# Performance work log

Measured on AMD Instinct MI355X. Metric: run time of the kernel, lower is better.

## Reference

```python
import jax, jax.numpy as jnp
import numpy as np

N = 50000
E = 800000
IN_DIM = 128
OUT_DIM = 128


def setup_inputs() -> dict:
    key = jax.random.key(0)
    k1, k2, k3, k4 = jax.random.split(key, 4)
    x = jax.random.normal(k1, (N, IN_DIM), dtype=jnp.float32)
    edge_index = jax.random.randint(k2, (2, E), 0, N, dtype=jnp.int64)
    # Linear(in_dim*2, out_dim) params
    W = jax.random.normal(k3, (2 * IN_DIM, OUT_DIM), dtype=jnp.float32) * (1.0 / np.sqrt(2 * IN_DIM))
    b = jax.random.normal(k4, (OUT_DIM,), dtype=jnp.float32) * 0.01
    return {"x": x, "edge_index": edge_index, "W": W, "b": b}


def reference(x, edge_index, W, b):
    src, dst = edge_index[0], edge_index[1]
    diff = x[src] - x[dst]                              # (E, C)
    # segment-max over destination nodes; empty segments get -inf identity
    seg_max = jax.ops.segment_max(diff, dst, num_segments=N)  # (N, C)
    counts = jax.ops.segment_sum(jnp.ones((E,), dtype=jnp.int32), dst, num_segments=N)
    # original code leaves zeros for nodes with no incoming edges
    max_diff = jnp.where((counts > 0)[:, None], seg_max, jnp.zeros_like(seg_max))
    x_cat = jnp.concatenate([x, max_diff], axis=-1)     # (N, 2C)
    return x_cat @ W + b
```

## Files before the change

### kernel.cpp

```cpp
#include <hip/hip_runtime.h>
#include <math.h>

#define NN 50000
#define NE 800000
#define CD 128
#define PB 3200

typedef __attribute__((ext_vector_type(8))) short short8;
typedef __attribute__((ext_vector_type(4))) float f32x4;
typedef unsigned long long ull;


__device__ inline unsigned pack2bf(float lo, float hi) {
    unsigned a = __float_as_uint(lo), b = __float_as_uint(hi);
    a = (a + 0x7fffu + ((a >> 16) & 1u)) >> 16;
    b = (b + 0x7fffu + ((b >> 16) & 1u)) & 0xffff0000u;
    return a | b;
}

__device__ inline unsigned short f2bf(float f) {
    unsigned u = __float_as_uint(f);
    return (unsigned short)((u + 0x7fffu + ((u >> 16) & 1u)) >> 16);
}

__device__ inline void fmax8(float* m, uint4 v) {
    m[0] = fmaxf(m[0], __uint_as_float(v.x << 16));
    m[1] = fmaxf(m[1], __uint_as_float(v.x & 0xffff0000u));
    m[2] = fmaxf(m[2], __uint_as_float(v.y << 16));
    m[3] = fmaxf(m[3], __uint_as_float(v.y & 0xffff0000u));
    m[4] = fmaxf(m[4], __uint_as_float(v.z << 16));
    m[5] = fmaxf(m[5], __uint_as_float(v.z & 0xffff0000u));
    m[6] = fmaxf(m[6], __uint_as_float(v.w << 16));
    m[7] = fmaxf(m[7], __uint_as_float(v.w & 0xffff0000u));
}


__global__ __launch_bounds__(256) void prep3_k(const int* __restrict__ ei,
                                               const float* __restrict__ x,
                                               const float* __restrict__ W,
                                               int* __restrict__ head,
                                               ull* __restrict__ nxt2,
                                               unsigned* __restrict__ xb,
                                               unsigned short* __restrict__ wt) {
    int tid0 = blockIdx.x * 256 + threadIdx.x;
    int phase = blockIdx.x & 1;

    for (int p = 0; p < 2; p++) {
        if ((p ^ phase) == 0) {
            for (int e = tid0; e < NE; e += PB * 256) {
                int d = ei[NE + e];
                unsigned s = (unsigned)ei[e];
                int old = atomicExch(&head[d], e);
                nxt2[e] = ((ull)s << 32) | (unsigned)old;
            }
        } else {
            for (int i = tid0; i < NN * CD / 4; i += PB * 256) {
                float4 v = ((const float4*)x)[i];
                uint2 r;
                r.x = pack2bf(v.x, v.y);
                r.y = pack2bf(v.z, v.w);
                ((uint2*)xb)[i] = r;
            }
        }
    }
    for (int i = tid0; i < 2 * CD * CD; i += PB * 256) {
        int n = i >> 8, k = i & 255;
        wt[(size_t)n * 256 + k] = f2bf(W[(size_t)k * 128 + n]);
    }
}


__global__ __launch_bounds__(512) void fused_k(const unsigned* __restrict__ xb,
                                               const int* __restrict__ head,
                                               const ull* __restrict__ nxt2,
                                               const short* __restrict__ wt,
                                               const float* __restrict__ bias,
                                               float* __restrict__ out) {
    __shared__ unsigned short idx[64][72];
    __shared__ unsigned short deg[64];
    __shared__ int ovf[64];
    __shared__ unsigned short amx[64][136];

    int t = threadIdx.x;
    int nbase = blockIdx.x * 64;

    if (t < 64) {
        int node = nbase + t;
        int e = (node < NN) ? head[node] : -1;
        int cnt = 0;
        while (e >= 0 && cnt < 64) {
            ull v = nxt2[e];
            idx[t][cnt] = (unsigned short)(v >> 32);
            e = (int)(unsigned)(v & 0xffffffffu);
            cnt++;
        }
        deg[t] = (unsigned short)cnt;
        ovf[t] = e;
    }
    __syncthreads();

    int w = t >> 6, lane = t & 63;
    int q = lane >> 4, c = lane & 15;
#pragma unroll 1
    for (int j = 0; j < 2; j++) {
        int ln = w * 8 + j * 4 + q;
        int node = nbase + ln;
        int cnt = deg[ln];
        float m[8];
#pragma unroll
        for (int i = 0; i < 8; i++) m[i] = -INFINITY;

        for (int base = 0; base < cnt; base += 8) {
            uint4 pk = *(const uint4*)&idx[ln][base];
            int s0 = (int)(pk.x & 0xffffu), s1 = (int)(pk.x >> 16);
            int s2 = (int)(pk.y & 0xffffu), s3 = (int)(pk.y >> 16);
            int s4 = (int)(pk.z & 0xffffu), s5 = (int)(pk.z >> 16);
            int s6 = (int)(pk.w & 0xffffu), s7 = (int)(pk.w >> 16);
            if (base + 8 <= cnt) {
                fmax8(m, *(const uint4*)(xb + (size_t)s0 * 64 + c * 4));
                fmax8(m, *(const uint4*)(xb + (size_t)s1 * 64 + c * 4));
                fmax8(m, *(const uint4*)(xb + (size_t)s2 * 64 + c * 4));
                fmax8(m, *(const uint4*)(xb + (size_t)s3 * 64 + c * 4));
                fmax8(m, *(const uint4*)(xb + (size_t)s4 * 64 + c * 4));
                fmax8(m, *(const uint4*)(xb + (size_t)s5 * 64 + c * 4));
                fmax8(m, *(const uint4*)(xb + (size_t)s6 * 64 + c * 4));
                fmax8(m, *(const uint4*)(xb + (size_t)s7 * 64 + c * 4));
            } else {
                if (base + 0 < cnt) fmax8(m, *(const uint4*)(xb + (size_t)s0 * 64 + c * 4));
                if (base + 1 < cnt) fmax8(m, *(const uint4*)(xb + (size_t)s1 * 64 + c * 4));
                if (base + 2 < cnt) fmax8(m, *(const uint4*)(xb + (size_t)s2 * 64 + c * 4));
                if (base + 3 < cnt) fmax8(m, *(const uint4*)(xb + (size_t)s3 * 64 + c * 4));
                if (base + 4 < cnt) fmax8(m, *(const uint4*)(xb + (size_t)s4 * 64 + c * 4));
                if (base + 5 < cnt) fmax8(m, *(const uint4*)(xb + (size_t)s5 * 64 + c * 4));
                if (base + 6 < cnt) fmax8(m, *(const uint4*)(xb + (size_t)s6 * 64 + c * 4));
                if (base + 7 < cnt) fmax8(m, *(const uint4*)(xb + (size_t)s7 * 64 + c * 4));
            }
        }
        int e = ovf[ln];
        while (e >= 0) {
            ull v = nxt2[e];
            int s = (int)(v >> 32);
            fmax8(m, *(const uint4*)(xb + (size_t)s * 64 + c * 4));
            e = (int)(unsigned)(v & 0xffffffffu);
        }
        uint4 r = make_uint4(0u, 0u, 0u, 0u);
        if (cnt > 0) {
            uint4 xd = *(const uint4*)(xb + (size_t)node * 64 + c * 4);
            float d0 = m[0] - __uint_as_float(xd.x << 16);
            float d1 = m[1] - __uint_as_float(xd.x & 0xffff0000u);
            float d2 = m[2] - __uint_as_float(xd.y << 16);
            float d3 = m[3] - __uint_as_float(xd.y & 0xffff0000u);
            float d4 = m[4] - __uint_as_float(xd.z << 16);
            float d5 = m[5] - __uint_as_float(xd.z & 0xffff0000u);
            float d6 = m[6] - __uint_as_float(xd.w << 16);
            float d7 = m[7] - __uint_as_float(xd.w & 0xffff0000u);
            r.x = pack2bf(d0, d1);
            r.y = pack2bf(d2, d3);
            r.z = pack2bf(d4, d5);
            r.w = pack2bf(d6, d7);
        }
        *(uint4*)&amx[ln][c * 8] = r;
    }
    __syncthreads();

    int mm = lane & 15, g = lane >> 4;
    int rt = w & 3, ch = w >> 2;
    int r0 = nbase + rt * 16;
    int row = r0 + mm;
    bool rowok = row < NN;

    f32x4 acc[4];
#pragma unroll
    for (int ct = 0; ct < 4; ct++) {
        float bv = bias[ch * 64 + ct * 16 + mm];
        acc[ct] = (f32x4){bv, bv, bv, bv};
    }

    const short* xbs = (const short*)xb;
#pragma unroll
    for (int kc = 0; kc < 8; kc++) {
        int k0 = kc * 32;
        short8 a;
        if (kc < 4) {
            a = (short8){0, 0, 0, 0, 0, 0, 0, 0};
            if (rowok) a = *(const short8*)(xbs + (size_t)row * 128 + k0 + g * 8);
        } else {
            a = *(const short8*)&amx[rt * 16 + mm][(k0 - 128) + g * 8];
        }
#pragma unroll
        for (int ct = 0; ct < 4; ct++) {
            short8 b = *(const short8*)(wt + (size_t)(ch * 64 + ct * 16 + mm) * 256 + k0 + g * 8);
            acc[ct] = __builtin_amdgcn_mfma_f32_16x16x32_bf16(a, b, acc[ct], 0, 0, 0);
        }
    }

#pragma unroll
    for (int ct = 0; ct < 4; ct++) {
#pragma unroll
        for (int i = 0; i < 4; i++) {
            int rr = r0 + g * 4 + i;
            if (rr < NN) out[(size_t)rr * 128 + ch * 64 + ct * 16 + mm] = acc[ct][i];
        }
    }
}


extern "C" void kernel_launch(void* const* d_in, const int* in_sizes, int n_in,
                              void* d_out, int out_size, void* d_ws, size_t ws_size,
                              hipStream_t stream) {
    const float* x = (const float*)d_in[0];
    const int* ei = (const int*)d_in[1];
    const float* W = (const float*)d_in[2];
    const float* bias = (const float*)d_in[3];
    float* out = (float*)d_out;

    int* wsi = (int*)d_ws;
    int* head = wsi;
    ull* nxt2 = (ull*)(wsi + 50048);
    unsigned* xb  = (unsigned*)(wsi + 1650048);
    unsigned short* wt = (unsigned short*)(wsi + 4850048);

    hipMemsetAsync(head, 0xFF, NN * sizeof(int), stream);

    prep3_k<<<PB, 256, 0, stream>>>(ei, x, W, head, nxt2, xb, wt);
    fused_k<<<(NN + 63) / 64, 512, 0, stream>>>(xb, head, nxt2, (const short*)wt,
                                                bias, out);
}
```

Measured before the change: 186.5 us.

## Replace per-edge linked lists with 32-node bucketed edge bins and overflow list

Result: slower. 193.1 us (+3.5%).

```diff
diff --git a/kernel.cpp b/kernel.cpp
--- a/kernel.cpp
+++ b/kernel.cpp
@@ -5,10 +5,12 @@
 #define NE 800000
 #define CD 128
 #define PB 3200
+#define NBLK 1563
+#define CSTR 1568
+#define SCAP 160
 
 typedef __attribute__((ext_vector_type(8))) short short8;
 typedef __attribute__((ext_vector_type(4))) float f32x4;
-typedef unsigned long long ull;
 
 
 __device__ inline unsigned pack2bf(float lo, float hi) {
@@ -35,23 +37,35 @@
 }
 
 
-__global__ __launch_bounds__(256) void prep3_k(const int* __restrict__ ei,
+__global__ __launch_bounds__(256) void prep4_k(const int* __restrict__ ei,
                                                const float* __restrict__ x,
                                                const float* __restrict__ W,
-                                               int* __restrict__ head,
-                                               ull* __restrict__ nxt2,
+                                               int* __restrict__ cur,
+                                               int* __restrict__ ovfn,
+                                               unsigned* __restrict__ ovf,
+                                               unsigned* __restrict__ ent,
                                                unsigned* __restrict__ xb,
                                                unsigned short* __restrict__ wt) {
-    int tid0 = blockIdx.x * 256 + threadIdx.x;
-    int phase = blockIdx.x & 1;
+    int t = threadIdx.x;
+    int b = blockIdx.x;
+    int tid0 = b * 256 + t;
+    int g = b & 7;
+    int phase = (b >> 3) & 1;
 
     for (int p = 0; p < 2; p++) {
         if ((p ^ phase) == 0) {
             for (int e = tid0; e < NE; e += PB * 256) {
                 int d = ei[NE + e];
-                unsigned s = (unsigned)ei[e];
-                int old = atomicExch(&head[d], e);
-                nxt2[e] = ((ull)s << 32) | (unsigned)old;
+                int s = ei[e];
+                int bin = d >> 5;
+                int pos = atomicAdd(&cur[g * CSTR + bin], 1);
+                if (pos < SCAP) {
+                    ent[(size_t)(g * NBLK + bin) * SCAP + pos] =
+                        ((unsigned)s << 6) | (unsigned)(d & 31);
+                } else {
+                    int op = atomicAdd(ovfn, 1);
+                    ovf[op] = ((unsigned)s << 16) | (unsigned)d;
+                }
             }
         } else {
             for (int i = tid0; i < NN * CD / 4; i += PB * 256) {
@@ -70,53 +84,74 @@
 }
 
 
-__global__ __launch_bounds__(512) void fused_k(const unsigned* __restrict__ xb,
-                                               const int* __restrict__ head,
-                                               const ull* __restrict__ nxt2,
+__global__ __launch_bounds__(256) void fused_k(const unsigned* __restrict__ xb,
+                                               const int* __restrict__ cur,
+                                               const int* __restrict__ ovfn,
+                                               const unsigned* __restrict__ ovf,
+                                               const unsigned* __restrict__ ent,
                                                const short* __restrict__ wt,
                                                const float* __restrict__ bias,
                                                float* __restrict__ out) {
-    __shared__ unsigned short idx[64][72];
-    __shared__ unsigned short deg[64];
-    __shared__ int ovf[64];
-    __shared__ unsigned short amx[64][136];
+    __shared__ unsigned short idx[32][72];
+    __shared__ unsigned short amx[32][136];
+    __shared__ int lcnt[32];
+    __shared__ int spill[512];
+    __shared__ int spn;
 
     int t = threadIdx.x;
-    int nbase = blockIdx.x * 64;
-
-    if (t < 64) {
-        int node = nbase + t;
-        int e = (node < NN) ? head[node] : -1;
-        int cnt = 0;
-        while (e >= 0 && cnt < 64) {
-            ull v = nxt2[e];
-            idx[t][cnt] = (unsigned short)(v >> 32);
-            e = (int)(unsigned)(v & 0xffffffffu);
-            cnt++;
-        }
-        deg[t] = (unsigned short)cnt;
-        ovf[t] = e;
+    int b = blockIdx.x;
+    int nbase = b * 32;
+
+    if (t < 32) lcnt[t] = 0;
+    if (t == 32) spn = 0;
+    __syncthreads();
+
+    for (int g = 0; g < 8; g++) {
+        int cnt = min(cur[g * CSTR + b], SCAP);
+        const unsigned* base = ent + (size_t)(g * NBLK + b) * SCAP;
+        if (t < cnt) {
+            unsigned w = base[t];
+            int ln = (int)(w & 31u);
+            int s = (int)(w >> 6);
+            int pos = atomicAdd(&lcnt[ln], 1);
+            if (pos < 64) idx[ln][pos] = (unsigned short)s;
+            else { int sp = atomicAdd(&spn, 1); if (sp < 512) spill[sp] = (s << 6) | ln; }
+        }
+    }
+    int ovN = min(ovfn[0], NE);
+    for (int i = t; i < ovN; i += 256) {
+        unsigned w = ovf[i];
+        int d = (int)(w & 0xffffu);
+        if ((d >> 5) == b) {
+            int ln = d & 31;
+            int s = (int)(w >> 16);
+            int pos = atomicAdd(&lcnt[ln], 1);
+            if (pos < 64) idx[ln][pos] = (unsigned short)s;
+            else { int sp = atomicAdd(&spn, 1); if (sp < 512) spill[sp] = (s << 6) | ln; }
+        }
     }
     __syncthreads();
 
     int w = t >> 6, lane = t & 63;
     int q = lane >> 4, c = lane & 15;
+    int sN = min(spn, 512);
 #pragma unroll 1
     for (int j = 0; j < 2; j++) {
         int ln = w * 8 + j * 4 + q;
         int node = nbase + ln;
-        int cnt = deg[ln];
+        int cnt = lcnt[ln];
+        int lim = min(cnt, 64);
         float m[8];
 #pragma unroll
         for (int i = 0; i < 8; i++) m[i] = -INFINITY;
 
-        for (int base = 0; base < cnt; base += 8) {
+        for (int base = 0; base < lim; base += 8) {
             uint4 pk = *(const uint4*)&idx[ln][base];
             int s0 = (int)(pk.x & 0xffffu), s1 = (int)(pk.x >> 16);
             int s2 = (int)(pk.y & 0xffffu), s3 = (int)(pk.y >> 16);
             int s4 = (int)(pk.z & 0xffffu), s5 = (int)(pk.z >> 16);
             int s6 = (int)(pk.w & 0xffffu), s7 = (int)(pk.w >> 16);
-            if (base + 8 <= cnt) {
+            if (base + 8 <= lim) {
                 fmax8(m, *(const uint4*)(xb + (size_t)s0 * 64 + c * 4));
                 fmax8(m, *(const uint4*)(xb + (size_t)s1 * 64 + c * 4));
                 fmax8(m, *(const uint4*)(xb + (size_t)s2 * 64 + c * 4));
@@ -126,22 +161,20 @@
                 fmax8(m, *(const uint4*)(xb + (size_t)s6 * 64 + c * 4));
                 fmax8(m, *(const uint4*)(xb + (size_t)s7 * 64 + c * 4));
             } else {
-                if (base + 0 < cnt) fmax8(m, *(const uint4*)(xb + (size_t)s0 * 64 + c * 4));
-                if (base + 1 < cnt) fmax8(m, *(const uint4*)(xb + (size_t)s1 * 64 + c * 4));
-                if (base + 2 < cnt) fmax8(m, *(const uint4*)(xb + (size_t)s2 * 64 + c * 4));
-                if (base + 3 < cnt) fmax8(m, *(const uint4*)(xb + (size_t)s3 * 64 + c * 4));
-                if (base + 4 < cnt) fmax8(m, *(const uint4*)(xb + (size_t)s4 * 64 + c * 4));
-                if (base + 5 < cnt) fmax8(m, *(const uint4*)(xb + (size_t)s5 * 64 + c * 4));
-                if (base + 6 < cnt) fmax8(m, *(const uint4*)(xb + (size_t)s6 * 64 + c * 4));
-                if (base + 7 < cnt) fmax8(m, *(const uint4*)(xb + (size_t)s7 * 64 + c * 4));
+                if (base + 0 < lim) fmax8(m, *(const uint4*)(xb + (size_t)s0 * 64 + c * 4));
+                if (base + 1 < lim) fmax8(m, *(const uint4*)(xb + (size_t)s1 * 64 + c * 4));
+                if (base + 2 < lim) fmax8(m, *(const uint4*)(xb + (size_t)s2 * 64 + c * 4));
+                if (base + 3 < lim) fmax8(m, *(const uint4*)(xb + (size_t)s3 * 64 + c * 4));
+                if (base + 4 < lim) fmax8(m, *(const uint4*)(xb + (size_t)s4 * 64 + c * 4));
+                if (base + 5 < lim) fmax8(m, *(const uint4*)(xb + (size_t)s5 * 64 + c * 4));
+                if (base + 6 < lim) fmax8(m, *(const uint4*)(xb + (size_t)s6 * 64 + c * 4));
+                if (base + 7 < lim) fmax8(m, *(const uint4*)(xb + (size_t)s7 * 64 + c * 4));
             }
         }
-        int e = ovf[ln];
-        while (e >= 0) {
-            ull v = nxt2[e];
-            int s = (int)(v >> 32);
-            fmax8(m, *(const uint4*)(xb + (size_t)s * 64 + c * 4));
-            e = (int)(unsigned)(v & 0xffffffffu);
+        for (int i = 0; i < sN; i++) {
+            int sw = spill[i];
+            if ((sw & 63) == ln)
+                fmax8(m, *(const uint4*)(xb + (size_t)(sw >> 6) * 64 + c * 4));
         }
         uint4 r = make_uint4(0u, 0u, 0u, 0u);
         if (cnt > 0) {
@@ -163,8 +196,8 @@
     }
     __syncthreads();
 
-    int mm = lane & 15, g = lane >> 4;
-    int rt = w & 3, ch = w >> 2;
+    int mm = lane & 15, g4 = lane >> 4;
+    int rt = w & 1, ch = w >> 1;
     int r0 = nbase + rt * 16;
     int row = r0 + mm;
     bool rowok = row < NN;
@@ -183,14 +216,14 @@
         short8 a;
         if (kc < 4) {
             a = (short8){0, 0, 0, 0, 0, 0, 0, 0};
-            if (rowok) a = *(const short8*)(xbs + (size_t)row * 128 + k0 + g * 8);
+            if (rowok) a = *(const short8*)(xbs + (size_t)row * 128 + k0 + g4 * 8);
         } else {
-            a = *(const short8*)&amx[rt * 16 + mm][(k0 - 128) + g * 8];
+            a = *(const short8*)&amx[rt * 16 + mm][(k0 - 128) + g4 * 8];
         }
 #pragma unroll
         for (int ct = 0; ct < 4; ct++) {
-            short8 b = *(const short8*)(wt + (size_t)(ch * 64 + ct * 16 + mm) * 256 + k0 + g * 8);
-            acc[ct] = __builtin_amdgcn_mfma_f32_16x16x32_bf16(a, b, acc[ct], 0, 0, 0);
+            short8 bb = *(const short8*)(wt + (size_t)(ch * 64 + ct * 16 + mm) * 256 + k0 + g4 * 8);
+            acc[ct] = __builtin_amdgcn_mfma_f32_16x16x32_bf16(a, bb, acc[ct], 0, 0, 0);
         }
     }
 
@@ -198,7 +231,7 @@
     for (int ct = 0; ct < 4; ct++) {
 #pragma unroll
         for (int i = 0; i < 4; i++) {
-            int rr = r0 + g * 4 + i;
+            int rr = r0 + g4 * 4 + i;
             if (rr < NN) out[(size_t)rr * 128 + ch * 64 + ct * 16 + mm] = acc[ct][i];
         }
     }
@@ -215,14 +248,16 @@
     float* out = (float*)d_out;
 
     int* wsi = (int*)d_ws;
-    int* head = wsi;
-    ull* nxt2 = (ull*)(wsi + 50048);
-    unsigned* xb  = (unsigned*)(wsi + 1650048);
-    unsigned short* wt = (unsigned short*)(wsi + 4850048);
-
-    hipMemsetAsync(head, 0xFF, NN * sizeof(int), stream);
-
-    prep3_k<<<PB, 256, 0, stream>>>(ei, x, W, head, nxt2, xb, wt);
-    fused_k<<<(NN + 63) / 64, 512, 0, stream>>>(xb, head, nxt2, (const short*)wt,
-                                                bias, out);
-}
+    int* cur   = wsi;
+    int* ovfn  = wsi + 12544;
+    unsigned* ovf = (unsigned*)(wsi + 12560);
+    unsigned* ent = (unsigned*)(wsi + 812560);
+    unsigned* xb  = (unsigned*)(wsi + 2813200);
+    unsigned short* wt = (unsigned short*)(wsi + 6013200);
+
+    hipMemsetAsync(cur, 0, (8 * CSTR + 16) * sizeof(int), stream);
+
+    prep4_k<<<PB, 256, 0, stream>>>(ei, x, W, cur, ovfn, ovf, ent, xb, wt);
+    fused_k<<<NBLK, 256, 0, stream>>>(xb, cur, ovfn, ovf, ent, (const short*)wt,
+                                      bias, out);
+}
```
